# Kernel tuning notes

Measured on AMD Instinct MI355X. Metric: run time of the kernel, lower is better.

Reference implementation:

```python
import jax, jax.numpy as jnp
import numpy as np

B, T = 8, 1024
C, H, K, FF, L = 512, 8, 64, 2048, 6
STATE, INP, NBINS, NACT, MAXT = 128, 128, 41, 16, 2048
EPS = 1e-5


def _ln(x, g, b):
    m = jnp.mean(x, axis=-1, keepdims=True)
    v = jnp.var(x, axis=-1, keepdims=True)
    return (x - m) / jnp.sqrt(v + EPS) * g + b


def setup_inputs() -> dict:
    key = jax.random.key(0)
    ks = jax.random.split(key, 24)
    s = 0.02
    d = {}
    d["obs"] = jax.random.normal(ks[0], (B, T, STATE), jnp.float32)
    d["action"] = jax.random.randint(ks[1], (B, T), 0, NACT)
    d["step"] = jax.random.randint(ks[2], (B, T), 0, MAXT)
    # embeddings / input projections
    d["W_obs"] = s * jax.random.normal(ks[3], (STATE, C), jnp.float32)
    d["b_obs"] = jnp.zeros((C,), jnp.float32)
    d["E_act"] = s * jax.random.normal(ks[4], (NACT, C), jnp.float32)
    d["W_traj"] = s * jax.random.normal(ks[5], (2 * C, C), jnp.float32)
    d["b_traj"] = jnp.zeros((C,), jnp.float32)
    d["E_time"] = s * jax.random.normal(ks[6], (MAXT, C), jnp.float32)
    # per-layer stacked params (scanned over leading L axis)
    d["Wq"] = s * jax.random.normal(ks[7], (L, H, C, K), jnp.float32)
    d["Wk"] = s * jax.random.normal(ks[8], (L, H, C, K), jnp.float32)
    d["Wv"] = s * jax.random.normal(ks[9], (L, H, C, K), jnp.float32)
    d["Wp"] = s * jax.random.normal(ks[10], (L, H * K, C), jnp.float32)
    d["bp"] = jnp.zeros((L, C), jnp.float32)
    d["W1"] = s * jax.random.normal(ks[11], (L, C, FF), jnp.float32)
    d["b1"] = jnp.zeros((L, FF), jnp.float32)
    d["W2"] = s * jax.random.normal(ks[12], (L, FF, C), jnp.float32)
    d["b2"] = jnp.zeros((L, C), jnp.float32)
    d["g1"] = jnp.ones((L, C), jnp.float32)
    d["be1"] = jnp.zeros((L, C), jnp.float32)
    d["g2"] = jnp.ones((L, C), jnp.float32)
    d["be2"] = jnp.zeros((L, C), jnp.float32)
    # final norm + heads
    d["gf"] = jnp.ones((C,), jnp.float32)
    d["bf"] = jnp.zeros((C,), jnp.float32)
    d["W_oh"] = s * jax.random.normal(ks[13], (C, INP), jnp.float32)
    d["b_oh"] = jnp.zeros((INP,), jnp.float32)
    d["W_rh"] = s * jax.random.normal(ks[14], (C, NBINS), jnp.float32)
    d["b_rh"] = jnp.zeros((NBINS,), jnp.float32)
    d["W_dh"] = s * jax.random.normal(ks[15], (C, 1), jnp.float32)
    d["b_dh"] = jnp.zeros((1,), jnp.float32)
    return d


def reference(obs, action, step, W_obs, b_obs, E_act, W_traj, b_traj, E_time,
              Wq, Wk, Wv, Wp, bp, W1, b1, W2, b2, g1, be1, g2, be2,
              gf, bf, W_oh, b_oh, W_rh, b_rh, W_dh, b_dh):
    Bc, Tc = obs.shape[0], obs.shape[1]
    obs_emb = obs @ W_obs + b_obs                      # [B,T,C]
    act_emb = E_act[action]                            # [B,T,C]
    token = jnp.concatenate([obs_emb, act_emb], -1) @ W_traj + b_traj
    x = token + E_time[step]                           # [B,T,C]

    causal = jnp.tril(jnp.ones((Tc, Tc), bool))        # [T,T]
    scale = 1.0 / jnp.sqrt(jnp.asarray(K, x.dtype))

    def block(x, p):
        wq, wk, wv, wp, bpl, w1, b1l, w2, b2l, ga, ba, gb, bb = p
        q = jnp.einsum('btc,hck->bhtk', x, wq)
        k = jnp.einsum('btc,hck->bhtk', x, wk)
        v = jnp.einsum('btc,hck->bhtk', x, wv)
        wei = jnp.einsum('bhtk,bhsk->bhts', q, k) * scale
        wei = jnp.where(causal, wei, -jnp.inf)
        att = jax.nn.softmax(wei, axis=-1)             # dropout off (eval)
        o = jnp.einsum('bhts,bhsk->bhtk', att, v)
        o = o.transpose(0, 2, 1, 3).reshape(Bc, Tc, H * K)  # head-wise concat
        y = o @ wp + bpl
        x = _ln(x + y, ga, ba)                         # post-norm, as in source
        y = jax.nn.relu(x @ w1 + b1l) @ w2 + b2l
        x = _ln(x + y, gb, bb)
        return x, None

    x, _ = jax.lax.scan(block, x, (Wq, Wk, Wv, Wp, bp, W1, b1, W2, b2, g1, be1, g2, be2))
    x = _ln(x, gf, bf)
    obs_logits = x @ W_oh + b_oh
    reward_logits = x @ W_rh + b_rh
    done_logits = x @ W_dh + b_dh
    return (obs_logits, reward_logits, done_logits)
```

## Files before the change

kernel.cpp:

```cpp
#include <hip/hip_runtime.h>
#include <hip/hip_bf16.h>


#define TSEQ 1024
#define BB   8
#define CDIM 512
#define HH   8
#define KHD  64
#define FFD  2048
#define LL   6
#define MROWS (BB*TSEQ)

typedef __hip_bfloat16 bf16;
typedef __attribute__((ext_vector_type(8))) short bf16x8;
typedef __attribute__((ext_vector_type(4))) short bf16x4;
typedef __attribute__((ext_vector_type(4))) float f32x4;

#define MFMA16K16(a,b,c) __builtin_amdgcn_mfma_f32_16x16x16bf16_1k(a,b,c,0,0,0)

static __device__ __forceinline__ short f2bf_bits(float x) {
    bf16 t = __float2bfloat16(x);
    return *reinterpret_cast<short*>(&t);
}
static __device__ __forceinline__ float bf2f(short b) {
    unsigned u = ((unsigned)(unsigned short)b) << 16;
    return __uint_as_float(u);
}

static __device__ __forceinline__ void gload_lds16(const bf16* g, short* l) {
    __builtin_amdgcn_global_load_lds(
        (__attribute__((address_space(1))) const void*)g,
        (__attribute__((address_space(3))) void*)l, 16, 0, 0);
}

struct PrepJob { const float* src; long dstOff; int nrows; int kd; int type; };
struct PrepArgs { PrepJob jobs[48]; };

__global__ void __launch_bounds__(256) prep_weights(PrepArgs args, bf16* __restrict__ wsb)
{
    PrepJob J = args.jobs[blockIdx.y];
    const int tilesK = (J.kd + 63) >> 6;
    const int tilesN = (J.nrows + 63) >> 6;
    const int t = blockIdx.x;
    if (t >= tilesK * tilesN) return;
    const int tn = t / tilesK, tk = t - tn * tilesK;
    const int n0 = tn << 6, k0 = tk << 6;

    __shared__ float tile[64][65];
    const int tid = threadIdx.x;
    const bool full = (J.type != 3) && (n0 + 64 <= J.nrows) && (k0 + 64 <= J.kd);

    if (full) {
        const int c4 = (tid & 15) * 4;
        const int r0 = tid >> 4;
#pragma unroll
        for (int i = 0; i < 4; ++i) {
            int kl = r0 + i * 16;
            int k = k0 + kl;
            const float* src;
            if (J.type == 0) src = J.src + (long)k * J.nrows + n0 + c4;
            else             src = J.src + ((long)(n0 >> 6) * J.kd + k) * 64 + c4;
            float4 v = *(const float4*)src;
            tile[kl][c4 + 0] = v.x; tile[kl][c4 + 1] = v.y;
            tile[kl][c4 + 2] = v.z; tile[kl][c4 + 3] = v.w;
        }
        __syncthreads();
        const int kq = (tid & 15) * 4;
        const int n1 = tid >> 4;
#pragma unroll
        for (int i = 0; i < 4; ++i) {
            int nl = n1 + i * 16;
            bf16x4 o;
#pragma unroll
            for (int j2 = 0; j2 < 4; ++j2) o[j2] = f2bf_bits(tile[kq + j2][nl]);
            *(bf16x4*)(wsb + J.dstOff + (long)(n0 + nl) * J.kd + k0 + kq) = o;
        }
    } else {
#pragma unroll
        for (int i = 0; i < 16; ++i) {
            int e = tid + i * 256;
            int kl = e >> 6, nl = e & 63;
            int k = k0 + kl, n = n0 + nl;
            float v = 0.f;
            if (J.type != 3 && k < J.kd && n < J.nrows) {
                if (J.type == 0) v = J.src[(long)k * J.nrows + n];
                else             v = J.src[((long)(n >> 6) * J.kd + k) * 64 + (n & 63)];
            }
            tile[kl][nl] = v;
        }
        __syncthreads();
#pragma unroll
        for (int i = 0; i < 16; ++i) {
            int e = tid + i * 256;
            int nl = e >> 6, kl = e & 63;
            int n = n0 + nl, k = k0 + kl;
            if (n < J.nrows && k < J.kd)
                wsb[J.dstOff + (long)n * J.kd + k] = __float2bfloat16(tile[kl][nl]);
        }
    }
}

__global__ void build_head_bias(const float* __restrict__ b_oh, const float* __restrict__ b_rh,
                                const float* __restrict__ b_dh, float* __restrict__ hb)
{
    int i = threadIdx.x;
    float v = 0.f;
    if (i < 128) v = b_oh[i];
    else if (i < 169) v = b_rh[i - 128];
    else if (i == 169) v = b_dh[0];
    hb[i] = v;
}

template<int TN, int BK, int OUTMODE, bool BIAS, bool RELU>
__global__ void __launch_bounds__(256) gemm_kernel(
    const bf16* __restrict__ A, const bf16* __restrict__ BT,
    void* __restrict__ Cout, const float* __restrict__ bias,
    int M, int N, int Kd)
{
    constexpr int NJ = TN / 32;
    constexpr int SL = BK / 8;
    constexpr int AI = (128 * BK) / (8 * 256);
    constexpr int BI = (TN  * BK) / (8 * 256);
    __shared__ short As[128 * BK];
    __shared__ short Bs[TN * BK];
    const int tid = threadIdx.x;
    const int lane = tid & 63;
    const int w = tid >> 6;
    const int wm = w >> 1, wn = w & 1;
    const int m0 = blockIdx.x * 128;
    const int n0 = blockIdx.y * TN;
    const int g = lane >> 4, lr = lane & 15;

    f32x4 acc[4][NJ] = {};

    for (int k0 = 0; k0 < Kd; k0 += BK) {
#pragma unroll
        for (int it = 0; it < AI; ++it) {
            int cbase = (w * AI + it) * 64;
            int c = cbase + lane;
            int row = c / SL, slot = c % SL;
            int ss = slot ^ (row & (SL - 1));
            gload_lds16(A + (size_t)(m0 + row) * Kd + k0 + ss * 8, As + cbase * 8);
        }
#pragma unroll
        for (int it = 0; it < BI; ++it) {
            int cbase = (w * BI + it) * 64;
            int c = cbase + lane;
            int row = c / SL, slot = c % SL;
            int ss = slot ^ (row & (SL - 1));
            gload_lds16(BT + (size_t)(n0 + row) * Kd + k0 + ss * 8, Bs + cbase * 8);
        }
        __syncthreads();
#pragma unroll
        for (int kk = 0; kk < BK; kk += 32) {
            bf16x8 af[4], bfr[NJ];
#pragma unroll
            for (int i = 0; i < 4; ++i) {
                int row = wm*64 + i*16 + lr;
                int ss = ((kk >> 3) + g) ^ (row & (SL - 1));
                af[i] = *(const bf16x8*)(As + row * BK + ss * 8);
            }
#pragma unroll
            for (int j = 0; j < NJ; ++j) {
                int row = wn*(TN/2) + j*16 + lr;
                int ss = ((kk >> 3) + g) ^ (row & (SL - 1));
                bfr[j] = *(const bf16x8*)(Bs + row * BK + ss * 8);
            }
#pragma unroll
            for (int i = 0; i < 4; ++i)
#pragma unroll
                for (int j = 0; j < NJ; ++j)
                    acc[i][j] = __builtin_amdgcn_mfma_f32_16x16x32_bf16(af[i], bfr[j], acc[i][j], 0, 0, 0);
        }
        __syncthreads();
    }

#pragma unroll
    for (int i = 0; i < 4; ++i) {
#pragma unroll
        for (int j = 0; j < NJ; ++j) {
            int col = n0 + wn*(TN/2) + j*16 + lr;
            float bv = 0.f;
            if (BIAS) bv = bias[col];
#pragma unroll
            for (int r = 0; r < 4; ++r) {
                int row = m0 + wm*64 + i*16 + g*4 + r;
                float v = acc[i][j][r] + bv;
                if (RELU) v = fmaxf(v, 0.f);
                if (OUTMODE == 1) {
                    ((bf16*)Cout)[(size_t)row * N + col] = __float2bfloat16(v);
                } else if (OUTMODE == 2) {
                    float* outf = (float*)Cout;
                    if (col < 128)      outf[(size_t)row * 128 + col] = v;
                    else if (col < 169) outf[1048576 + (size_t)row * 41 + (col - 128)] = v;
                    else if (col == 169) outf[1384448 + (size_t)row] = v;
                } else {
                    ((float*)Cout)[(size_t)row * N + col] = v;
                }
            }
        }
    }
}

__global__ void __launch_bounds__(256) attn_kernel(const bf16* __restrict__ qkv, bf16* __restrict__ o)
{
    const int bh = blockIdx.x;
    const int z  = blockIdx.y;
    const int b = bh >> 3, h = bh & 7;
    const int tid = threadIdx.x, lane = tid & 63, w = tid >> 6;
    const int g = lane >> 4, lr = lane & 15;
    const int qlo = z, qhi = 15 - z;
    const float SCL = 0.125f * 1.44269504089f;

    __shared__ short Ks[128][72];
    __shared__ short Vs[8192];

    const size_t base = (size_t)b * TSEQ * 1536;

    bf16x8 qfL[2], qfH[2];
#pragma unroll
    for (int kk = 0; kk < 2; ++kk) {
        qfL[kk] = *(const bf16x8*)(qkv + base + (size_t)(qlo*64 + w*16 + lr) * 1536 + h*64 + kk*32 + g*8);
        qfH[kk] = *(const bf16x8*)(qkv + base + (size_t)(qhi*64 + w*16 + lr) * 1536 + h*64 + kk*32 + g*8);
    }

    f32x4 accL[4] = {}, accH[4] = {};
    float mL = -1e30f, lL = 0.f, mH = -1e30f, lH = 0.f;

    const short* vtr = &Vs[lane * 4];

    auto proc = [&](const bf16x8* qf, f32x4* acc, float& m, float& l, int qt, int kt) {
        f32x4 st[8];
        __builtin_amdgcn_s_setprio(1);
#pragma unroll
        for (int j = 0; j < 8; ++j) {
            st[j] = f32x4{0.f, 0.f, 0.f, 0.f};
#pragma unroll
            for (int kk = 0; kk < 2; ++kk) {
                bf16x8 af = *(const bf16x8*)(&Ks[j*16 + lr][kk*32 + g*8]);
                st[j] = __builtin_amdgcn_mfma_f32_16x16x32_bf16(af, qf[kk], st[j], 0, 0, 0);
            }
        }
        __builtin_amdgcn_s_setprio(0);
        const int qg = qt*64 + w*16 + lr;
        const bool diag = (kt == (qt >> 1));
        float vmax = -1e30f;
#pragma unroll
        for (int j = 0; j < 8; ++j)
#pragma unroll
            for (int r = 0; r < 4; ++r) {
                float v = st[j][r] * SCL;
                if (diag && (kt*128 + j*16 + g*4 + r) > qg) v = -1e30f;
                st[j][r] = v;
                vmax = fmaxf(vmax, v);
            }
        vmax = fmaxf(vmax, __shfl_xor(vmax, 16));
        vmax = fmaxf(vmax, __shfl_xor(vmax, 32));
        if (!__all(vmax <= m + 8.f)) {
            float mn = fmaxf(m, vmax);
            float alpha = exp2f(m - mn);
            l *= alpha;
            float av[4];
#pragma unroll
            for (int r = 0; r < 4; ++r) av[r] = __shfl(alpha, g*4 + r);
#pragma unroll
            for (int dj = 0; dj < 4; ++dj)
#pragma unroll
                for (int r = 0; r < 4; ++r) acc[dj][r] *= av[r];
            m = mn;
        }
        float psum = 0.f;
        bf16x4 pf[8];
#pragma unroll
        for (int j = 0; j < 8; ++j)
#pragma unroll
            for (int r = 0; r < 4; ++r) {
                float p = exp2f(st[j][r] - m);
                psum += p;
                pf[j][r] = f2bf_bits(p);
            }
        psum += __shfl_xor(psum, 16);
        psum += __shfl_xor(psum, 32);
        l += psum;
#pragma unroll
        for (int half = 0; half < 4; ++half) {
            bf16x4 vf[2][4];
#pragma unroll
            for (int jj = 0; jj < 2; ++jj)
#pragma unroll
                for (int dj = 0; dj < 4; ++dj) {
                    asm volatile("ds_read_b64_tr_b16 %0, %1"
                        : "=v"(vf[jj][dj])
                        : "v"((const __attribute__((address_space(3))) short*)
                              (vtr + ((half*2 + jj)*4 + dj) * 256)));
                }
            asm volatile("s_waitcnt lgkmcnt(0)" ::: "memory");
            __builtin_amdgcn_sched_barrier(0);
            __builtin_amdgcn_s_setprio(1);
#pragma unroll
            for (int jj = 0; jj < 2; ++jj)
#pragma unroll
                for (int dj = 0; dj < 4; ++dj)
                    acc[dj] = MFMA16K16(pf[half*2 + jj], vf[jj][dj], acc[dj]);
            __builtin_amdgcn_s_setprio(0);
        }
    };

    const int ktmax = qhi >> 1;
    for (int kt = 0; kt <= ktmax; ++kt) {
#pragma unroll
        for (int it = 0; it < 4; ++it) {
            int idx = tid + it * 256;
            int row = idx >> 3;
            int col = (idx & 7) << 3;
            *(bf16x8*)(&Ks[row][col]) =
                *(const bf16x8*)(qkv + base + (size_t)(kt*128 + row)*1536 + 512 + h*64 + col);
            bf16x8 vv = *(const bf16x8*)(qkv + base + (size_t)(kt*128 + row)*1536 + 1024 + h*64 + col);
            int dst = ((row >> 4)*4 + (col >> 4))*256 + (row & 15)*16 + (col & 8);
            *(bf16x8*)(&Vs[dst]) = vv;
        }
        __syncthreads();
        proc(qfH, accH, mH, lH, qhi, kt);
        if (kt <= (qlo >> 1)) proc(qfL, accL, mL, lL, qlo, kt);
        __syncthreads();
    }

    auto wout = [&](const f32x4* acc, float l, int qt) {
        float linv = 1.f / l;
        float lv[4];
#pragma unroll
        for (int r = 0; r < 4; ++r) lv[r] = __shfl(linv, g*4 + r);
#pragma unroll
        for (int dj = 0; dj < 4; ++dj)
#pragma unroll
            for (int r = 0; r < 4; ++r) {
                int trow = qt*64 + w*16 + g*4 + r;
                o[((size_t)(b*TSEQ + trow))*512 + h*64 + dj*16 + lr] =
                    __float2bfloat16(acc[dj][r] * lv[r]);
            }
    };
    wout(accH, lH, qhi);
    wout(accL, lL, qlo);
}

template<bool HAS_RES>
__global__ void __launch_bounds__(256) ln_kernel(
    const bf16* __restrict__ y_, const bf16* __restrict__ xin,
    bf16* __restrict__ xb,
    const float* __restrict__ gamma, const float* __restrict__ beta)
{
    int row = blockIdx.x * 4 + (threadIdx.x >> 6);
    int lane = threadIdx.x & 63;
    int c0 = lane * 8;
    size_t rb = (size_t)row * CDIM + c0;
    float u[8];
    bf16x8 yv = *(const bf16x8*)(y_ + rb);
#pragma unroll
    for (int i = 0; i < 8; ++i) u[i] = bf2f(yv[i]);
    if (HAS_RES) {
        bf16x8 xv = *(const bf16x8*)(xin + rb);
#pragma unroll
        for (int i = 0; i < 8; ++i) u[i] += bf2f(xv[i]);
    }
    float s = 0.f, sq = 0.f;
#pragma unroll
    for (int i = 0; i < 8; ++i) { s += u[i]; sq += u[i]*u[i]; }
#pragma unroll
    for (int off = 1; off < 64; off <<= 1) { s += __shfl_xor(s, off); sq += __shfl_xor(sq, off); }
    float mean = s * (1.f / 512.f);
    float var  = sq * (1.f / 512.f) - mean * mean;
    float rstd = rsqrtf(var + 1e-5f);
    float4 g0 = *(const float4*)(gamma + c0);
    float4 g1 = *(const float4*)(gamma + c0 + 4);
    float4 be0 = *(const float4*)(beta + c0);
    float4 be1v = *(const float4*)(beta + c0 + 4);
    float gv[8] = {g0.x,g0.y,g0.z,g0.w,g1.x,g1.y,g1.z,g1.w};
    float bv[8] = {be0.x,be0.y,be0.z,be0.w,be1v.x,be1v.y,be1v.z,be1v.w};
    bf16x8 ob;
#pragma unroll
    for (int i = 0; i < 8; ++i)
        ob[i] = f2bf_bits((u[i] - mean) * rstd * gv[i] + bv[i]);
    *(bf16x8*)(xb + rb) = ob;
}

__global__ void __launch_bounds__(256) obs_convert(const float* __restrict__ obs, bf16* __restrict__ out)
{
    int idx = (blockIdx.x * 256 + threadIdx.x) * 4;
    float4 v = *(const float4*)(obs + idx);
    bf16x4 o = { f2bf_bits(v.x), f2bf_bits(v.y), f2bf_bits(v.z), f2bf_bits(v.w) };
    *(bf16x4*)(out + idx) = o;
}

__global__ void __launch_bounds__(256) concat_kernel(
    const bf16* __restrict__ obs_emb, const int* __restrict__ action,
    const float* __restrict__ E_act, bf16* __restrict__ cc)
{
    int row = blockIdx.x;
    int a = action[row];
    int c = threadIdx.x * 4;
    if (c < 512) {
        *(bf16x4*)(cc + (size_t)row * 1024 + c) =
            *(const bf16x4*)(obs_emb + (size_t)row * 512 + c);
    } else {
        float4 v = *(const float4*)(E_act + (size_t)a * 512 + (c - 512));
        bf16x4 o = { f2bf_bits(v.x), f2bf_bits(v.y), f2bf_bits(v.z), f2bf_bits(v.w) };
        *(bf16x4*)(cc + (size_t)row * 1024 + c) = o;
    }
}

__global__ void __launch_bounds__(256) xinit_kernel(
    const bf16* __restrict__ tok, const int* __restrict__ step,
    const float* __restrict__ E_time, bf16* __restrict__ xb)
{
    int row = blockIdx.x * 2 + (threadIdx.x >> 7);
    int c = (threadIdx.x & 127) * 4;
    int st = step[row];
    bf16x4 tv = *(const bf16x4*)(tok + (size_t)row * 512 + c);
    float4 ev = *(const float4*)(E_time + (size_t)st * 512 + c);
    bf16x4 o = { f2bf_bits(bf2f(tv[0]) + ev.x), f2bf_bits(bf2f(tv[1]) + ev.y),
                 f2bf_bits(bf2f(tv[2]) + ev.z), f2bf_bits(bf2f(tv[3]) + ev.w) };
    *(bf16x4*)(xb + (size_t)row * 512 + c) = o;
}

extern "C" void kernel_launch(void* const* d_in, const int* in_sizes, int n_in,
                              void* d_out, int out_size, void* d_ws, size_t ws_size,
                              hipStream_t stream)
{
    const float* obs    = (const float*)d_in[0];
    const int*   action = (const int*)  d_in[1];
    const int*   step   = (const int*)  d_in[2];
    const float* W_obs  = (const float*)d_in[3];
    const float* b_obs  = (const float*)d_in[4];
    const float* E_act  = (const float*)d_in[5];
    const float* W_traj = (const float*)d_in[6];
    const float* b_traj = (const float*)d_in[7];
    const float* E_time = (const float*)d_in[8];
    const float* Wq  = (const float*)d_in[9];
    const float* Wk  = (const float*)d_in[10];
    const float* Wv  = (const float*)d_in[11];
    const float* Wp  = (const float*)d_in[12];
    const float* bp  = (const float*)d_in[13];
    const float* W1  = (const float*)d_in[14];
    const float* b1  = (const float*)d_in[15];
    const float* W2  = (const float*)d_in[16];
    const float* b2  = (const float*)d_in[17];
    const float* g1  = (const float*)d_in[18];
    const float* be1 = (const float*)d_in[19];
    const float* g2  = (const float*)d_in[20];
    const float* be2 = (const float*)d_in[21];
    const float* gf  = (const float*)d_in[22];
    const float* bfp = (const float*)d_in[23];
    const float* W_oh = (const float*)d_in[24];
    const float* b_oh = (const float*)d_in[25];
    const float* W_rh = (const float*)d_in[26];
    const float* b_rh = (const float*)d_in[27];
    const float* W_dh = (const float*)d_in[28];
    const float* b_dh = (const float*)d_in[29];

    char* ws  = (char*)d_ws;
    bf16* wsb = (bf16*)ws;

    long off = 0;
    const long oWT_obs  = off; off += 512L * 128;
    const long oWT_traj = off; off += 512L * 1024;
    const long oWT_qkv  = off; off += 6L * 1536 * 512;
    const long oWT_p    = off; off += 6L * 512 * 512;
    const long oWT_1    = off; off += 6L * 2048 * 512;
    const long oWT_2    = off; off += 6L * 512 * 2048;
    const long oWT_hd   = off; off += 256L * 512;
    size_t byteOff = ((size_t)off * 2 + 255) & ~(size_t)255;

    auto take = [&](size_t bytes) {
        void* p = ws + byteOff;
        byteOff = (byteOff + bytes + 255) & ~(size_t)255;
        return p;
    };
    float* head_bias = (float*)take(256 * 4);
    bf16*  xb   = (bf16*) take((size_t)MROWS * 512 * 2);
    bf16*  qkv  = (bf16*) take((size_t)MROWS * 1536 * 2);
    bf16*  o    = (bf16*) take((size_t)MROWS * 512 * 2);
    bf16*  hbuf = (bf16*) take((size_t)MROWS * 2048 * 2);
    (void)ws_size; (void)in_sizes; (void)n_in; (void)out_size;

    PrepArgs pa;
    int nj = 0;
    auto addJob = [&](const float* src, long dstOff, int nrows, int kd, int type) {
        pa.jobs[nj].src = src; pa.jobs[nj].dstOff = dstOff;
        pa.jobs[nj].nrows = nrows; pa.jobs[nj].kd = kd; pa.jobs[nj].type = type; ++nj;
    };
    addJob(W_obs,  oWT_obs,  512, 128,  0);
    addJob(W_traj, oWT_traj, 512, 1024, 0);
    for (int l = 0; l < 6; ++l) {
        long qb = oWT_qkv + (long)l * 1536 * 512;
        addJob(Wq + (long)l * 8 * 512 * 64, qb,               512, 512, 1);
        addJob(Wk + (long)l * 8 * 512 * 64, qb + 512L * 512,  512, 512, 1);
        addJob(Wv + (long)l * 8 * 512 * 64, qb + 1024L * 512, 512, 512, 1);
        addJob(Wp + (long)l * 512 * 512,  oWT_p + (long)l * 512 * 512,  512,  512,  0);
        addJob(W1 + (long)l * 512 * 2048, oWT_1 + (long)l * 2048 * 512, 2048, 512,  0);
        addJob(W2 + (long)l * 2048 * 512, oWT_2 + (long)l * 512 * 2048, 512,  2048, 0);
    }
    addJob(W_oh, oWT_hd,             128, 512, 0);
    addJob(W_rh, oWT_hd + 128L*512,  41,  512, 0);
    addJob(W_dh, oWT_hd + 169L*512,  1,   512, 0);
    addJob(nullptr, oWT_hd + 170L*512, 86, 512, 3);

    prep_weights<<<dim3(256, nj), 256, 0, stream>>>(pa, wsb);
    build_head_bias<<<1, 256, 0, stream>>>(b_oh, b_rh, b_dh, head_bias);

    bf16* obs_bf = o;
    obs_convert<<<(MROWS * 128) / 1024, 256, 0, stream>>>(obs, obs_bf);
    bf16* obs_emb = qkv;
    gemm_kernel<64, 128, 1, true, false><<<dim3(64, 8), 256, 0, stream>>>(
        obs_bf, wsb + oWT_obs, obs_emb, b_obs, MROWS, 512, 128);
    bf16* cc = hbuf;
    concat_kernel<<<MROWS, 256, 0, stream>>>(obs_emb, action, E_act, cc);
    bf16* tok = o;
    gemm_kernel<64, 128, 1, true, false><<<dim3(64, 8), 256, 0, stream>>>(
        cc, wsb + oWT_traj, tok, b_traj, MROWS, 512, 1024);
    xinit_kernel<<<MROWS / 2, 256, 0, stream>>>(tok, step, E_time, xb);

    for (int l = 0; l < 6; ++l) {
        gemm_kernel<128, 64, 1, false, false><<<dim3(64, 12), 256, 0, stream>>>(
            xb, wsb + oWT_qkv + (long)l * 1536 * 512, qkv, nullptr, MROWS, 1536, 512);
        attn_kernel<<<dim3(64, 8), 256, 0, stream>>>(qkv, o);
        gemm_kernel<64, 128, 1, true, false><<<dim3(64, 8), 256, 0, stream>>>(
            o, wsb + oWT_p + (long)l * 512 * 512, hbuf, bp + (long)l * 512, MROWS, 512, 512);
        ln_kernel<true><<<MROWS / 4, 256, 0, stream>>>(
            hbuf, xb, xb, g1 + l * 512, be1 + l * 512);
        gemm_kernel<128, 64, 1, true, true><<<dim3(64, 16), 256, 0, stream>>>(
            xb, wsb + oWT_1 + (long)l * 2048 * 512, hbuf, b1 + l * 2048, MROWS, 2048, 512);
        gemm_kernel<64, 128, 1, true, false><<<dim3(64, 8), 256, 0, stream>>>(
            hbuf, wsb + oWT_2 + (long)l * 512 * 2048, o, b2 + l * 512, MROWS, 512, 2048);
        ln_kernel<true><<<MROWS / 4, 256, 0, stream>>>(
            o, xb, xb, g2 + l * 512, be2 + l * 512);
    }

    ln_kernel<false><<<MROWS / 4, 256, 0, stream>>>(
        xb, nullptr, xb, gf, bfp);
    gemm_kernel<64, 128, 2, true, false><<<dim3(64, 4), 256, 0, stream>>>(
        xb, wsb + oWT_hd, d_out, head_bias, MROWS, 256, 512);
}
```

Measured before the change: 811.7 us.

## Fuse residual adds and time embedding into GEMM epilogues, add 256x256 FFN1 GEMM

Residual addition moves out of the layernorm kernel into the projection and FFN2 GEMM epilogues, and the time-embedding gather moves into the trajectory GEMM epilogue, which removes the xinit kernel. This saves one full activation read per layernorm and one elementwise pass. A new 256x256-tile, 512-thread GEMM using 16x16x32 bf16 MFMA handles the FFN1 projection to raise data reuse. The risks are the epilogue's uncoalesced residual reads and lower occupancy from the large-tile kernel.

```diff
diff --git a/kernel.cpp b/kernel.cpp
--- a/kernel.cpp
+++ b/kernel.cpp
@@ -115,7 +115,8 @@
 __global__ void __launch_bounds__(256) gemm_kernel(
     const bf16* __restrict__ A, const bf16* __restrict__ BT,
     void* __restrict__ Cout, const float* __restrict__ bias,
-    int M, int N, int Kd)
+    int M, int N, int Kd,
+    const void* __restrict__ aux1, const float* __restrict__ aux2)
 {
     constexpr int NJ = TN / 32;
     constexpr int SL = BK / 8;
@@ -194,9 +195,95 @@
                     if (col < 128)      outf[(size_t)row * 128 + col] = v;
                     else if (col < 169) outf[1048576 + (size_t)row * 41 + (col - 128)] = v;
                     else if (col == 169) outf[1384448 + (size_t)row] = v;
+                } else if (OUTMODE == 3) {
+                    const bf16* res = (const bf16*)aux1;
+                    v += bf2f(*(const short*)(res + (size_t)row * N + col));
+                    ((bf16*)Cout)[(size_t)row * N + col] = __float2bfloat16(v);
+                } else if (OUTMODE == 4) {
+                    const int* stp = (const int*)aux1;
+                    v += aux2[(size_t)stp[row] * 512 + col];
+                    ((bf16*)Cout)[(size_t)row * N + col] = __float2bfloat16(v);
                 } else {
                     ((float*)Cout)[(size_t)row * N + col] = v;
                 }
+            }
+        }
+    }
+}
+
+template<bool BIAS, bool RELU>
+__global__ void __launch_bounds__(512) gemm256_kernel(
+    const bf16* __restrict__ A, const bf16* __restrict__ BT,
+    bf16* __restrict__ Cout, const float* __restrict__ bias,
+    int M, int N, int Kd)
+{
+    __shared__ short As[256 * 64];
+    __shared__ short Bs[256 * 64];
+    const int tid = threadIdx.x;
+    const int lane = tid & 63;
+    const int w = tid >> 6;
+    const int wr = w >> 2, wc = w & 3;
+    const int m0 = blockIdx.x * 256;
+    const int n0 = blockIdx.y * 256;
+    const int g = lane >> 4, lr = lane & 15;
+
+    f32x4 acc[8][4] = {};
+
+    for (int k0 = 0; k0 < Kd; k0 += 64) {
+#pragma unroll
+        for (int it = 0; it < 4; ++it) {
+            int cbase = (w * 4 + it) * 64;
+            int c = cbase + lane;
+            int row = c >> 3, slot = c & 7;
+            int ss = slot ^ (row & 7);
+            gload_lds16(A + (size_t)(m0 + row) * Kd + k0 + ss * 8, As + cbase * 8);
+        }
+#pragma unroll
+        for (int it = 0; it < 4; ++it) {
+            int cbase = (w * 4 + it) * 64;
+            int c = cbase + lane;
+            int row = c >> 3, slot = c & 7;
+            int ss = slot ^ (row & 7);
+            gload_lds16(BT + (size_t)(n0 + row) * Kd + k0 + ss * 8, Bs + cbase * 8);
+        }
+        __syncthreads();
+#pragma unroll
+        for (int kk = 0; kk < 64; kk += 32) {
+            bf16x8 af[8], bfr[4];
+#pragma unroll
+            for (int i = 0; i < 8; ++i) {
+                int row = wr*128 + i*16 + lr;
+                int ss = ((kk >> 3) + g) ^ (row & 7);
+                af[i] = *(const bf16x8*)(As + row * 64 + ss * 8);
+            }
+#pragma unroll
+            for (int j = 0; j < 4; ++j) {
+                int row = wc*64 + j*16 + lr;
+                int ss = ((kk >> 3) + g) ^ (row & 7);
+                bfr[j] = *(const bf16x8*)(Bs + row * 64 + ss * 8);
+            }
+#pragma unroll
+            for (int i = 0; i < 8; ++i)
+#pragma unroll
+                for (int j = 0; j < 4; ++j)
+                    acc[i][j] = __builtin_amdgcn_mfma_f32_16x16x32_bf16(af[i], bfr[j], acc[i][j], 0, 0, 0);
+        }
+        __syncthreads();
+    }
+
+#pragma unroll
+    for (int i = 0; i < 8; ++i) {
+#pragma unroll
+        for (int j = 0; j < 4; ++j) {
+            int col = n0 + wc*64 + j*16 + lr;
+            float bv = 0.f;
+            if (BIAS) bv = bias[col];
+#pragma unroll
+            for (int r = 0; r < 4; ++r) {
+                int row = m0 + wr*128 + i*16 + g*4 + r;
+                float v = acc[i][j][r] + bv;
+                if (RELU) v = fmaxf(v, 0.f);
+                Cout[(size_t)row * N + col] = __float2bfloat16(v);
             }
         }
     }
@@ -343,10 +430,8 @@
     wout(accL, lL, qlo);
 }
 
-template<bool HAS_RES>
 __global__ void __launch_bounds__(256) ln_kernel(
-    const bf16* __restrict__ y_, const bf16* __restrict__ xin,
-    bf16* __restrict__ xb,
+    const bf16* __restrict__ u_, bf16* __restrict__ xb,
     const float* __restrict__ gamma, const float* __restrict__ beta)
 {
     int row = blockIdx.x * 4 + (threadIdx.x >> 6);
@@ -354,14 +439,9 @@
     int c0 = lane * 8;
     size_t rb = (size_t)row * CDIM + c0;
     float u[8];
-    bf16x8 yv = *(const bf16x8*)(y_ + rb);
+    bf16x8 yv = *(const bf16x8*)(u_ + rb);
 #pragma unroll
     for (int i = 0; i < 8; ++i) u[i] = bf2f(yv[i]);
-    if (HAS_RES) {
-        bf16x8 xv = *(const bf16x8*)(xin + rb);
-#pragma unroll
-        for (int i = 0; i < 8; ++i) u[i] += bf2f(xv[i]);
-    }
     float s = 0.f, sq = 0.f;
 #pragma unroll
     for (int i = 0; i < 8; ++i) { s += u[i]; sq += u[i]*u[i]; }
@@ -406,20 +486,6 @@
         bf16x4 o = { f2bf_bits(v.x), f2bf_bits(v.y), f2bf_bits(v.z), f2bf_bits(v.w) };
         *(bf16x4*)(cc + (size_t)row * 1024 + c) = o;
     }
-}
-
-__global__ void __launch_bounds__(256) xinit_kernel(
-    const bf16* __restrict__ tok, const int* __restrict__ step,
-    const float* __restrict__ E_time, bf16* __restrict__ xb)
-{
-    int row = blockIdx.x * 2 + (threadIdx.x >> 7);
-    int c = (threadIdx.x & 127) * 4;
-    int st = step[row];
-    bf16x4 tv = *(const bf16x4*)(tok + (size_t)row * 512 + c);
-    float4 ev = *(const float4*)(E_time + (size_t)st * 512 + c);
-    bf16x4 o = { f2bf_bits(bf2f(tv[0]) + ev.x), f2bf_bits(bf2f(tv[1]) + ev.y),
-                 f2bf_bits(bf2f(tv[2]) + ev.z), f2bf_bits(bf2f(tv[3]) + ev.w) };
-    *(bf16x4*)(xb + (size_t)row * 512 + c) = o;
 }
 
 extern "C" void kernel_launch(void* const* d_in, const int* in_sizes, int n_in,
@@ -511,32 +577,28 @@
     obs_convert<<<(MROWS * 128) / 1024, 256, 0, stream>>>(obs, obs_bf);
     bf16* obs_emb = qkv;
     gemm_kernel<64, 128, 1, true, false><<<dim3(64, 8), 256, 0, stream>>>(
-        obs_bf, wsb + oWT_obs, obs_emb, b_obs, MROWS, 512, 128);
+        obs_bf, wsb + oWT_obs, obs_emb, b_obs, MROWS, 512, 128, nullptr, nullptr);
     bf16* cc = hbuf;
     concat_kernel<<<MROWS, 256, 0, stream>>>(obs_emb, action, E_act, cc);
-    bf16* tok = o;
-    gemm_kernel<64, 128, 1, true, false><<<dim3(64, 8), 256, 0, stream>>>(
-        cc, wsb + oWT_traj, tok, b_traj, MROWS, 512, 1024);
-    xinit_kernel<<<MROWS / 2, 256, 0, stream>>>(tok, step, E_time, xb);
+    gemm_kernel<64, 128, 4, true, false><<<dim3(64, 8), 256, 0, stream>>>(
+        cc, wsb + oWT_traj, xb, b_traj, MROWS, 512, 1024, step, E_time);
 
     for (int l = 0; l < 6; ++l) {
         gemm_kernel<128, 64, 1, false, false><<<dim3(64, 12), 256, 0, stream>>>(
-            xb, wsb + oWT_qkv + (long)l * 1536 * 512, qkv, nullptr, MROWS, 1536, 512);
+            xb, wsb + oWT_qkv + (long)l * 1536 * 512, qkv, nullptr, MROWS, 1536, 512, nullptr, nullptr);
         attn_kernel<<<dim3(64, 8), 256, 0, stream>>>(qkv, o);
-        gemm_kernel<64, 128, 1, true, false><<<dim3(64, 8), 256, 0, stream>>>(
-            o, wsb + oWT_p + (long)l * 512 * 512, hbuf, bp + (long)l * 512, MROWS, 512, 512);
-        ln_kernel<true><<<MROWS / 4, 256, 0, stream>>>(
-            hbuf, xb, xb, g1 + l * 512, be1 + l * 512);
-        gemm_kernel<128, 64, 1, true, true><<<dim3(64, 16), 256, 0, stream>>>(
+        bf16* u1 = qkv;
+        gemm_kernel<64, 128, 3, true, false><<<dim3(64, 8), 256, 0, stream>>>(
+            o, wsb + oWT_p + (long)l * 512 * 512, u1, bp + (long)l * 512, MROWS, 512, 512, xb, nullptr);
+        ln_kernel<<<MROWS / 4, 256, 0, stream>>>(u1, xb, g1 + l * 512, be1 + l * 512);
+        gemm256_kernel<true, true><<<dim3(32, 8), 512, 0, stream>>>(
             xb, wsb + oWT_1 + (long)l * 2048 * 512, hbuf, b1 + l * 2048, MROWS, 2048, 512);
-        gemm_kernel<64, 128, 1, true, false><<<dim3(64, 8), 256, 0, stream>>>(
-            hbuf, wsb + oWT_2 + (long)l * 512 * 2048, o, b2 + l * 512, MROWS, 512, 2048);
-        ln_kernel<true><<<MROWS / 4, 256, 0, stream>>>(
-            o, xb, xb, g2 + l * 512, be2 + l * 512);
-    }
-
-    ln_kernel<false><<<MROWS / 4, 256, 0, stream>>>(
-        xb, nullptr, xb, gf, bfp);
+        gemm_kernel<64, 128, 3, true, false><<<dim3(64, 8), 256, 0, stream>>>(
+            hbuf, wsb + oWT_2 + (long)l * 512 * 2048, o, b2 + l * 512, MROWS, 512, 2048, xb, nullptr);
+        ln_kernel<<<MROWS / 4, 256, 0, stream>>>(o, xb, g2 + l * 512, be2 + l * 512);
+    }
+
+    ln_kernel<<<MROWS / 4, 256, 0, stream>>>(xb, xb, gf, bfp);
     gemm_kernel<64, 128, 2, true, false><<<dim3(64, 4), 256, 0, stream>>>(
-        xb, wsb + oWT_hd, d_out, head_bias, MROWS, 256, 512);
-}
+        xb, wsb + oWT_hd, d_out, head_bias, MROWS, 256, 512, nullptr, nullptr);
+}
```

Result: slower. 833.6 us (+2.7%).
